# Kernel tuning notes

Hardware: AMD Instinct MI355X
Metric: run time of the kernel (lower is better)

## Reference

```python
import jax, jax.numpy as jnp
import numpy as np

B, T, F, H = 64, 2048, 128, 32  # batch, seq_len, input_features, lstm hidden


def setup_inputs() -> dict:
    key = jax.random.key(0)
    ks = jax.random.split(key, 4)
    X = jax.random.normal(ks[0], (B, T, F), dtype=jnp.float32)
    # combined gate weights, order (i, f, g, o) as in flax.linen.LSTMCell
    Wx = jax.random.normal(ks[1], (F, 4 * H), dtype=jnp.float32) / np.float32(np.sqrt(F))
    Wh = jax.random.normal(ks[2], (H, 4 * H), dtype=jnp.float32) / np.float32(np.sqrt(H))
    b = jnp.zeros((4 * H,), dtype=jnp.float32)
    Wd = jax.random.normal(ks[3], (H, 1), dtype=jnp.float32) / np.float32(np.sqrt(H))
    bd = jnp.zeros((1,), dtype=jnp.float32)
    return {"X": X, "Wx": Wx, "Wh": Wh, "b": b, "Wd": Wd, "bd": bd}


def reference(X, Wx, Wh, b, Wd, bd):
    # Precompute input->gate projections for all timesteps in one GEMM.
    xg = jnp.einsum('btf,fg->btg', X, Wx) + b  # [B, T, 4H]

    def step(carry, xg_t):
        c, h = carry
        g = xg_t + h @ Wh  # [B, 4H]
        i, f, gc, o = jnp.split(g, 4, axis=-1)
        c = jax.nn.sigmoid(f) * c + jax.nn.sigmoid(i) * jnp.tanh(gc)
        h = jax.nn.sigmoid(o) * jnp.tanh(c)
        return (c, h), None

    zeros = jnp.zeros((X.shape[0], H), X.dtype)
    (c_T, h_T), _ = jax.lax.scan(step, (zeros, zeros), jnp.swapaxes(xg, 0, 1))
    # Dense(1) applied to outputs, then last timestep selected == Dense on h_T
    return h_T @ Wd + bd  # [B, 1]
```

## Files before the change

kernel.cpp:

```cpp
#include <hip/hip_runtime.h>
#include <math.h>

#define BB 64
#define TT 2048
#define FF 128
#define HH 32
#define GG 128

#define S1f (-1.4426950408889634f)
#define S2f (-2.8853900817779268f)

typedef _Float16 half2_t __attribute__((ext_vector_type(2)));

__device__ __forceinline__ unsigned h2u(half2_t v) {
    unsigned u; __builtin_memcpy(&u, &v, 4); return u;
}
__device__ __forceinline__ half2_t u2h(unsigned u) {
    half2_t v; __builtin_memcpy(&v, &u, 4); return v;
}
__device__ __forceinline__ half2_t pkrtz(float a, float b) {
    auto r = __builtin_amdgcn_cvt_pkrtz(a, b);
    half2_t v; __builtin_memcpy(&v, &r, 4); return v;
}
__device__ __forceinline__ float rcp_(float x) { return __builtin_amdgcn_rcpf(x); }
__device__ __forceinline__ float exp2_(float x) { return __builtin_amdgcn_exp2f(x); }
__device__ __forceinline__ float fdot2_(half2_t a, half2_t b, float c) {
    return __builtin_amdgcn_fdot2(a, b, c, false);
}

#define DPP_(x, ctrl) \
    ((unsigned)__builtin_amdgcn_mov_dpp((int)(x), (ctrl), 0xF, 0xF, true))
#define CTRL_XOR1 0xB1
#define CTRL_XOR2 0x4E
#define SWZ16_(x) ((unsigned)__builtin_amdgcn_ds_swizzle((int)(x), 0x401F))

#if __has_builtin(__builtin_amdgcn_permlane16_swap)
#define HAVE_PL16 1
#else
#define HAVE_PL16 0
#endif

__device__ __forceinline__ void gather_tree(unsigned v0, unsigned g[16]) {
#if HAVE_PL16
    unsigned v1 = DPP_(v0, CTRL_XOR2);
    auto sw = __builtin_amdgcn_permlane16_swap(v0, v1, false, false);
    unsigned s0 = (unsigned)sw[0], s1 = (unsigned)sw[1];
#else
    unsigned s0 = v0;
    unsigned s1 = SWZ16_(v0);
#endif
    g[0] = s0;                 g[1] = s1;
    g[2]  = DPP_(s0, 0x122);   g[3]  = DPP_(s1, 0x122);
    g[4]  = DPP_(s0, 0x124);   g[5]  = DPP_(s1, 0x124);
    g[6]  = DPP_(s0, 0x126);   g[7]  = DPP_(s1, 0x126);
    g[8]  = DPP_(s0, 0x128);   g[9]  = DPP_(s1, 0x128);
    g[10] = DPP_(s0, 0x12A);   g[11] = DPP_(s1, 0x12A);
    g[12] = DPP_(s0, 0x12C);   g[13] = DPP_(s1, 0x12C);
    g[14] = DPP_(s0, 0x12E);   g[15] = DPP_(s1, 0x12E);
}

__global__ __launch_bounds__(256) void xg_gemm(const float* __restrict__ X,
                                               const float* __restrict__ Wx,
                                               const float* __restrict__ bias,
                                               unsigned* __restrict__ xg2) {
    __shared__ unsigned XLh[64][16];
    __shared__ unsigned WLh[16][128];
    const int tid = threadIdx.x;
    const int row0 = blockIdx.x * 64;
    const int j0 = (tid & 15) * 4;
    const int r0 = (tid >> 4) * 4;

    float acc[4][8];
#pragma unroll
    for (int r = 0; r < 4; ++r)
#pragma unroll
        for (int jj = 0; jj < 8; ++jj) acc[r][jj] = 0.f;

    for (int f0 = 0; f0 < FF; f0 += 32) {
        __syncthreads();
        {
            const int jq = (tid & 31) * 4;
#pragma unroll
            for (int qq = 0; qq < 2; ++qq) {
                const int q = (tid >> 5) + qq * 8;
                float4 wa = *(const float4*)(Wx + (size_t)(f0 + 2 * q) * GG + jq);
                float4 wb = *(const float4*)(Wx + (size_t)(f0 + 2 * q + 1) * GG + jq);
                WLh[q][jq + 0] = h2u(pkrtz(wa.x, wb.x));
                WLh[q][jq + 1] = h2u(pkrtz(wa.y, wb.y));
                WLh[q][jq + 2] = h2u(pkrtz(wa.z, wb.z));
                WLh[q][jq + 3] = h2u(pkrtz(wa.w, wb.w));
            }
        }
        {
            int lin = tid * 4;
            int row = lin >> 5, fi = lin & 31;
            float4 x = *(const float4*)(X + (size_t)(row0 + row) * FF + f0 + fi);
            XLh[row][(fi >> 1) + 0] = h2u(pkrtz(x.x, x.y));
            XLh[row][(fi >> 1) + 1] = h2u(pkrtz(x.z, x.w));
            lin = (tid + 256) * 4;
            row = lin >> 5; fi = lin & 31;
            x = *(const float4*)(X + (size_t)(row0 + row) * FF + f0 + fi);
            XLh[row][(fi >> 1) + 0] = h2u(pkrtz(x.x, x.y));
            XLh[row][(fi >> 1) + 1] = h2u(pkrtz(x.z, x.w));
        }
        __syncthreads();
#pragma unroll 4
        for (int q = 0; q < 16; ++q) {
            half2_t xv[4];
#pragma unroll
            for (int r = 0; r < 4; ++r) xv[r] = u2h(XLh[r0 + r][q]);
            uint4 w0 = *(uint4*)&WLh[q][j0];
            uint4 w1 = *(uint4*)&WLh[q][j0 + 64];
            unsigned wj[8] = {w0.x, w0.y, w0.z, w0.w, w1.x, w1.y, w1.z, w1.w};
#pragma unroll
            for (int r = 0; r < 4; ++r)
#pragma unroll
                for (int jj = 0; jj < 8; ++jj)
                    acc[r][jj] = fdot2_(xv[r], u2h(wj[jj]), acc[r][jj]);
        }
    }
    const int b  = row0 >> 11;
    const int t0 = (row0 & 2047) + r0;
#pragma unroll
    for (int jj = 0; jj < 4; ++jj) {
        const int j = j0 + jj;
        const float bX = bias[j];
        const float bY = bias[j + 64];
        const float sY = (j < 32) ? S2f : S1f;
        uint4 o;
        o.x = h2u(pkrtz((acc[0][jj] + bX) * S1f, (acc[0][jj + 4] + bY) * sY));
        o.y = h2u(pkrtz((acc[1][jj] + bX) * S1f, (acc[1][jj + 4] + bY) * sY));
        o.z = h2u(pkrtz((acc[2][jj] + bX) * S1f, (acc[2][jj + 4] + bY) * sY));
        o.w = h2u(pkrtz((acc[3][jj] + bX) * S1f, (acc[3][jj + 4] + bY) * sY));
        *(uint4*)(xg2 + (size_t)(b * 64 + j) * TT + t0) = o;
    }
}

__global__ __launch_bounds__(64) void lstm_rec(const unsigned* __restrict__ xg2,
                                               const float* __restrict__ Wh,
                                               const float* __restrict__ Wd,
                                               const float* __restrict__ bd,
                                               float* __restrict__ out) {
    const int l = threadIdx.x;
    const int m = l & 31;
    const bool lo = (l < HH);
    const int b = blockIdx.x;

    unsigned iv[16];
    gather_tree((unsigned)m, iv);

    const float scx = S1f;
    const float scy = lo ? S2f : S1f;
    half2_t whx[16], why[16];
#pragma unroll
    for (int r = 0; r < 16; ++r) {
        const int p  = (int)(iv[r] & 31u);
        const int p2 = p ^ 1;
        whx[r] = pkrtz(Wh[p * GG + l] * scx,       Wh[p2 * GG + l] * scx);
        why[r] = pkrtz(Wh[p * GG + l + 64] * scy,  Wh[p2 * GG + l + 64] * scy);
    }

    const float A1 = lo ? 2.f : 1.f;
    const float B1 = lo ? -1.f : 0.f;

    float h = 0.f;
    float c = 0.f;

    const unsigned* pX = xg2 + (size_t)(b * 64 + l) * TT;

    uint4 cur = *(const uint4*)(pX);
    uint4 nxt = *(const uint4*)(pX + 4);

    auto step = [&](unsigned w) __attribute__((always_inline)) {
        half2_t xv = u2h(w);
        float xi = (float)xv[0];
        float xy = (float)xv[1];
        unsigned hn = DPP_(__float_as_uint(h), CTRL_XOR1);
        unsigned g0 = h2u(pkrtz(h, __uint_as_float(hn)));
        unsigned g[16];
        gather_tree(g0, g);
        float ax[4] = {xi, 0.f, 0.f, 0.f};
        float ay[4] = {xy, 0.f, 0.f, 0.f};
#pragma unroll
        for (int r = 0; r < 16; ++r) {
            half2_t hp = u2h(g[r]);
            ax[r & 3] = fdot2_(hp, whx[r], ax[r & 3]);
            ay[r & 3] = fdot2_(hp, why[r], ay[r & 3]);
        }
        float a0 = (ax[0] + ax[1]) + (ax[2] + ax[3]);
        float a1 = (ay[0] + ay[1]) + (ay[2] + ay[3]);
        float act0 = rcp_(1.f + exp2_(a0));
        float act1 = fmaf(A1, rcp_(1.f + exp2_(a1)), B1);
        auto sw0 = __builtin_amdgcn_permlane32_swap(__float_as_uint(act0),
                                                    __float_as_uint(act0), false, false);
        auto sw1 = __builtin_amdgcn_permlane32_swap(__float_as_uint(act1),
                                                    __float_as_uint(act1), false, false);
        float i_all = __uint_as_float(sw0[0]);
        float f_all = __uint_as_float(sw0[1]);
        float g_all = __uint_as_float(sw1[0]);
        float o_all = __uint_as_float(sw1[1]);
        c = fmaf(f_all, c, i_all * g_all);
        float tc = fmaf(2.f, rcp_(1.f + exp2_(c * S2f)), -1.f);
        h = o_all * tc;
    };

#pragma unroll 1
    for (int t4 = 0; t4 < TT; t4 += 4) {
        uint4 u = cur;
        cur = nxt;
        if (t4 + 8 < TT) nxt = *(const uint4*)(pX + t4 + 8);
        step(u.x);
        step(u.y);
        step(u.z);
        step(u.w);
    }

    float contrib = h * Wd[m];
#pragma unroll
    for (int off = 32; off >= 1; off >>= 1)
        contrib += __shfl_xor(contrib, off, 64);
    if (l == 0) out[b] = fmaf(0.5f, contrib, bd[0]);
}

extern "C" void kernel_launch(void* const* d_in, const int* in_sizes, int n_in,
                              void* d_out, int out_size, void* d_ws, size_t ws_size,
                              hipStream_t stream) {
    const float* X    = (const float*)d_in[0];
    const float* Wx   = (const float*)d_in[1];
    const float* Wh   = (const float*)d_in[2];
    const float* bias = (const float*)d_in[3];
    const float* Wd   = (const float*)d_in[4];
    const float* bd   = (const float*)d_in[5];
    float* out = (float*)d_out;
    unsigned* xg2 = (unsigned*)d_ws;

    hipLaunchKernelGGL(xg_gemm, dim3((BB * TT) / 64), dim3(256), 0, stream,
                       X, Wx, bias, xg2);
    hipLaunchKernelGGL(lstm_rec, dim3(BB), dim3(64), 0, stream,
                       xg2, Wh, Wd, bd, out);
}
```

Baseline: 454.5 us.

## Interleave two independent batch recurrences per wavefront to hide dependency latency

Each wavefront now advances two batch elements' LSTM recurrences together, and the launch uses half as many blocks. The two chains' DPP shuffles, dot products, transcendentals and permlane swaps are interleaved, so the latency of each serial step can overlap with the other chain's independent work. Empty inline-asm register barriers are added to pin the instruction order against compiler rescheduling. The cost is more VGPRs and twice the work per step for each wave, with only 32 waves running on a device that has many CUs.

Result: slower. 756.0 us (+66.3%).

```diff
diff --git a/kernel.cpp b/kernel.cpp
--- a/kernel.cpp
+++ b/kernel.cpp
@@ -39,6 +39,12 @@
 #else
 #define HAVE_PL16 0
 #endif
+
+#define LAD2(a, b) asm volatile("" : "+v"(a), "+v"(b))
+#define LAD4(a, b, c, d) asm volatile("" : "+v"(a), "+v"(b), "+v"(c), "+v"(d))
+#define LAD8(a, b, c, d, e, f, g, h) \
+    asm volatile("" : "+v"(a), "+v"(b), "+v"(c), "+v"(d), \
+                      "+v"(e), "+v"(f), "+v"(g), "+v"(h))
 
 __device__ __forceinline__ void gather_tree(unsigned v0, unsigned g[16]) {
 #if HAVE_PL16
@@ -144,7 +150,7 @@
     const int l = threadIdx.x;
     const int m = l & 31;
     const bool lo = (l < HH);
-    const int b = blockIdx.x;
+    const int b0 = blockIdx.x * 2;
 
     unsigned iv[16];
     gather_tree((unsigned)m, iv);
@@ -163,63 +169,156 @@
     const float A1 = lo ? 2.f : 1.f;
     const float B1 = lo ? -1.f : 0.f;
 
-    float h = 0.f;
-    float c = 0.f;
-
-    const unsigned* pX = xg2 + (size_t)(b * 64 + l) * TT;
-
-    uint4 cur = *(const uint4*)(pX);
-    uint4 nxt = *(const uint4*)(pX + 4);
-
-    auto step = [&](unsigned w) __attribute__((always_inline)) {
-        half2_t xv = u2h(w);
-        float xi = (float)xv[0];
-        float xy = (float)xv[1];
-        unsigned hn = DPP_(__float_as_uint(h), CTRL_XOR1);
-        unsigned g0 = h2u(pkrtz(h, __uint_as_float(hn)));
-        unsigned g[16];
-        gather_tree(g0, g);
-        float ax[4] = {xi, 0.f, 0.f, 0.f};
-        float ay[4] = {xy, 0.f, 0.f, 0.f};
-#pragma unroll
-        for (int r = 0; r < 16; ++r) {
-            half2_t hp = u2h(g[r]);
-            ax[r & 3] = fdot2_(hp, whx[r], ax[r & 3]);
-            ay[r & 3] = fdot2_(hp, why[r], ay[r & 3]);
-        }
-        float a0 = (ax[0] + ax[1]) + (ax[2] + ax[3]);
-        float a1 = (ay[0] + ay[1]) + (ay[2] + ay[3]);
-        float act0 = rcp_(1.f + exp2_(a0));
-        float act1 = fmaf(A1, rcp_(1.f + exp2_(a1)), B1);
-        auto sw0 = __builtin_amdgcn_permlane32_swap(__float_as_uint(act0),
-                                                    __float_as_uint(act0), false, false);
-        auto sw1 = __builtin_amdgcn_permlane32_swap(__float_as_uint(act1),
-                                                    __float_as_uint(act1), false, false);
-        float i_all = __uint_as_float(sw0[0]);
-        float f_all = __uint_as_float(sw0[1]);
-        float g_all = __uint_as_float(sw1[0]);
-        float o_all = __uint_as_float(sw1[1]);
-        c = fmaf(f_all, c, i_all * g_all);
-        float tc = fmaf(2.f, rcp_(1.f + exp2_(c * S2f)), -1.f);
-        h = o_all * tc;
+    float hA = 0.f, cA = 0.f, hB = 0.f, cB = 0.f;
+
+    const unsigned* pA = xg2 + (size_t)(b0 * 64 + l) * TT;
+    const unsigned* pB = xg2 + (size_t)((b0 + 1) * 64 + l) * TT;
+
+    uint4 curA = *(const uint4*)(pA);
+    uint4 curB = *(const uint4*)(pB);
+    uint4 nxtA = *(const uint4*)(pA + 4);
+    uint4 nxtB = *(const uint4*)(pB + 4);
+
+    auto dual_step = [&](unsigned wA, unsigned wB)
+        __attribute__((always_inline)) {
+        unsigned hnA = DPP_(__float_as_uint(hA), CTRL_XOR1);
+        unsigned hnB = DPP_(__float_as_uint(hB), CTRL_XOR1);
+        unsigned g0A = h2u(pkrtz(hA, __uint_as_float(hnA)));
+        unsigned g0B = h2u(pkrtz(hB, __uint_as_float(hnB)));
+#if HAVE_PL16
+        unsigned v1A = DPP_(g0A, CTRL_XOR2);
+        unsigned v1B = DPP_(g0B, CTRL_XOR2);
+        auto swA = __builtin_amdgcn_permlane16_swap(g0A, v1A, false, false);
+        auto swB = __builtin_amdgcn_permlane16_swap(g0B, v1B, false, false);
+        unsigned s0A = (unsigned)swA[0], s1A = (unsigned)swA[1];
+        unsigned s0B = (unsigned)swB[0], s1B = (unsigned)swB[1];
+#else
+        unsigned s0A = g0A, s1A = SWZ16_(g0A);
+        unsigned s0B = g0B, s1B = SWZ16_(g0B);
+#endif
+        LAD4(s0A, s1A, s0B, s1B);
+
+        half2_t xvA = u2h(wA);
+        half2_t xvB = u2h(wB);
+        float axA[4] = {(float)xvA[0], 0.f, 0.f, 0.f};
+        float ayA[4] = {(float)xvA[1], 0.f, 0.f, 0.f};
+        float axB[4] = {(float)xvB[0], 0.f, 0.f, 0.f};
+        float ayB[4] = {(float)xvB[1], 0.f, 0.f, 0.f};
+        {
+            half2_t hA0 = u2h(s0A), hA1 = u2h(s1A);
+            half2_t hB0 = u2h(s0B), hB1 = u2h(s1B);
+            axA[0] = fdot2_(hA0, whx[0], axA[0]);
+            axB[0] = fdot2_(hB0, whx[0], axB[0]);
+            ayA[0] = fdot2_(hA0, why[0], ayA[0]);
+            ayB[0] = fdot2_(hB0, why[0], ayB[0]);
+            axA[1] = fdot2_(hA1, whx[1], axA[1]);
+            axB[1] = fdot2_(hB1, whx[1], axB[1]);
+            ayA[1] = fdot2_(hA1, why[1], ayA[1]);
+            ayB[1] = fdot2_(hB1, why[1], ayB[1]);
+        }
+        LAD8(axA[0], ayA[0], axB[0], ayB[0], axA[1], ayA[1], axB[1], ayB[1]);
+
+#define ROR_LEVEL(CTRL, R)                                                  \
+        {                                                                   \
+            unsigned gA0 = DPP_(s0A, (CTRL));                               \
+            unsigned gA1 = DPP_(s1A, (CTRL));                               \
+            unsigned gB0 = DPP_(s0B, (CTRL));                               \
+            unsigned gB1 = DPP_(s1B, (CTRL));                               \
+            axA[(R) & 3] = fdot2_(u2h(gA0), whx[(R)], axA[(R) & 3]);        \
+            axB[(R) & 3] = fdot2_(u2h(gB0), whx[(R)], axB[(R) & 3]);        \
+            ayA[(R) & 3] = fdot2_(u2h(gA0), why[(R)], ayA[(R) & 3]);        \
+            ayB[(R) & 3] = fdot2_(u2h(gB0), why[(R)], ayB[(R) & 3]);        \
+            axA[((R) + 1) & 3] = fdot2_(u2h(gA1), whx[(R) + 1], axA[((R) + 1) & 3]); \
+            axB[((R) + 1) & 3] = fdot2_(u2h(gB1), whx[(R) + 1], axB[((R) + 1) & 3]); \
+            ayA[((R) + 1) & 3] = fdot2_(u2h(gA1), why[(R) + 1], ayA[((R) + 1) & 3]); \
+            ayB[((R) + 1) & 3] = fdot2_(u2h(gB1), why[(R) + 1], ayB[((R) + 1) & 3]); \
+        }
+
+        ROR_LEVEL(0x122, 2)
+        ROR_LEVEL(0x124, 4)
+        LAD8(axA[0], ayA[1], axB[0], ayB[1], axA[2], ayA[3], axB[2], ayB[3]);
+        ROR_LEVEL(0x126, 6)
+        ROR_LEVEL(0x128, 8)
+        LAD8(axA[0], ayA[1], axB[0], ayB[1], axA[2], ayA[3], axB[2], ayB[3]);
+        ROR_LEVEL(0x12A, 10)
+        ROR_LEVEL(0x12C, 12)
+        ROR_LEVEL(0x12E, 14)
+        LAD8(axA[0], ayA[1], axB[0], ayB[1], axA[2], ayA[3], axB[2], ayB[3]);
+#undef ROR_LEVEL
+
+        float a0A = (axA[0] + axA[1]) + (axA[2] + axA[3]);
+        float a0B = (axB[0] + axB[1]) + (axB[2] + axB[3]);
+        float a1A = (ayA[0] + ayA[1]) + (ayA[2] + ayA[3]);
+        float a1B = (ayB[0] + ayB[1]) + (ayB[2] + ayB[3]);
+        LAD4(a0A, a1A, a0B, a1B);
+
+        float e0A = exp2_(a0A);
+        float e0B = exp2_(a0B);
+        float e1A = exp2_(a1A);
+        float e1B = exp2_(a1B);
+        LAD4(e0A, e1A, e0B, e1B);
+        float act0A = rcp_(1.f + e0A);
+        float act0B = rcp_(1.f + e0B);
+        float act1A = fmaf(A1, rcp_(1.f + e1A), B1);
+        float act1B = fmaf(A1, rcp_(1.f + e1B), B1);
+        LAD4(act0A, act1A, act0B, act1B);
+
+        auto sw0A = __builtin_amdgcn_permlane32_swap(__float_as_uint(act0A),
+                                                     __float_as_uint(act0A), false, false);
+        auto sw0B = __builtin_amdgcn_permlane32_swap(__float_as_uint(act0B),
+                                                     __float_as_uint(act0B), false, false);
+        auto sw1A = __builtin_amdgcn_permlane32_swap(__float_as_uint(act1A),
+                                                     __float_as_uint(act1A), false, false);
+        auto sw1B = __builtin_amdgcn_permlane32_swap(__float_as_uint(act1B),
+                                                     __float_as_uint(act1B), false, false);
+        float iA = __uint_as_float(sw0A[0]);
+        float fA = __uint_as_float(sw0A[1]);
+        float gA = __uint_as_float(sw1A[0]);
+        float oA = __uint_as_float(sw1A[1]);
+        float iB = __uint_as_float(sw0B[0]);
+        float fB = __uint_as_float(sw0B[1]);
+        float gB = __uint_as_float(sw1B[0]);
+        float oB = __uint_as_float(sw1B[1]);
+        LAD8(iA, fA, gA, oA, iB, fB, gB, oB);
+        cA = fmaf(fA, cA, iA * gA);
+        cB = fmaf(fB, cB, iB * gB);
+        LAD2(cA, cB);
+        float ecA = exp2_(cA * S2f);
+        float ecB = exp2_(cB * S2f);
+        LAD2(ecA, ecB);
+        float tcA = fmaf(2.f, rcp_(1.f + ecA), -1.f);
+        float tcB = fmaf(2.f, rcp_(1.f + ecB), -1.f);
+        hA = oA * tcA;
+        hB = oB * tcB;
+        LAD4(hA, cA, hB, cB);
     };
 
 #pragma unroll 1
     for (int t4 = 0; t4 < TT; t4 += 4) {
-        uint4 u = cur;
-        cur = nxt;
-        if (t4 + 8 < TT) nxt = *(const uint4*)(pX + t4 + 8);
-        step(u.x);
-        step(u.y);
-        step(u.z);
-        step(u.w);
-    }
-
-    float contrib = h * Wd[m];
-#pragma unroll
-    for (int off = 32; off >= 1; off >>= 1)
-        contrib += __shfl_xor(contrib, off, 64);
-    if (l == 0) out[b] = fmaf(0.5f, contrib, bd[0]);
+        uint4 uA = curA, uB = curB;
+        curA = nxtA; curB = nxtB;
+        if (t4 + 8 < TT) {
+            nxtA = *(const uint4*)(pA + t4 + 8);
+            nxtB = *(const uint4*)(pB + t4 + 8);
+        }
+        dual_step(uA.x, uB.x);
+        dual_step(uA.y, uB.y);
+        dual_step(uA.z, uB.z);
+        dual_step(uA.w, uB.w);
+    }
+
+    const float wd = Wd[m];
+    float ca = hA * wd;
+    float cb = hB * wd;
+#pragma unroll
+    for (int off = 32; off >= 1; off >>= 1) {
+        ca += __shfl_xor(ca, off, 64);
+        cb += __shfl_xor(cb, off, 64);
+    }
+    if (l == 0) {
+        out[b0]     = fmaf(0.5f, ca, bd[0]);
+        out[b0 + 1] = fmaf(0.5f, cb, bd[0]);
+    }
 }
 
 extern "C" void kernel_launch(void* const* d_in, const int* in_sizes, int n_in,
@@ -236,6 +335,6 @@
 
     hipLaunchKernelGGL(xg_gemm, dim3((BB * TT) / 64), dim3(256), 0, stream,
                        X, Wx, bias, xg2);
-    hipLaunchKernelGGL(lstm_rec, dim3(BB), dim3(64), 0, stream,
+    hipLaunchKernelGGL(lstm_rec, dim3(BB / 2), dim3(64), 0, stream,
                        xg2, Wh, Wd, bd, out);
 }
```

## Fuse input GEMM and LSTM recurrence with flag-based producer/consumer tiling

Applied to the files above, without the earlier changes.

Merges the two launches into one kernel. Blocks 0-63 act as producers, each computing the input projection for one batch row in 32 time tiles and publishing a per-tile flag with release semantics. Blocks 64-127 run the recurrence and acquire-poll the next tile's flag before consuming it, so the GEMM overlaps the serial scan instead of finishing first. The catch is a memset per call and the risk of deadlock if consumer blocks get scheduled ahead of producers; producers also use only 64 blocks, which lowers GEMM parallelism.

Result: slower. 596.0 us (+31.1%).

```diff
diff --git a/kernel.cpp b/kernel.cpp
--- a/kernel.cpp
+++ b/kernel.cpp
@@ -6,6 +6,8 @@
 #define FF 128
 #define HH 32
 #define GG 128
+#define NTILE 32
+#define FLAG_OFF (48u * 1024u * 1024u)
 
 #define S1f (-1.4426950408889634f)
 #define S2f (-2.8853900817779268f)
@@ -59,92 +61,110 @@
     g[14] = DPP_(s0, 0x12E);   g[15] = DPP_(s1, 0x12E);
 }
 
-__global__ __launch_bounds__(256) void xg_gemm(const float* __restrict__ X,
-                                               const float* __restrict__ Wx,
-                                               const float* __restrict__ bias,
-                                               unsigned* __restrict__ xg2) {
-    __shared__ unsigned XLh[64][16];
-    __shared__ unsigned WLh[16][128];
-    const int tid = threadIdx.x;
-    const int row0 = blockIdx.x * 64;
-    const int j0 = (tid & 15) * 4;
-    const int r0 = (tid >> 4) * 4;
-
-    float acc[4][8];
-#pragma unroll
-    for (int r = 0; r < 4; ++r)
-#pragma unroll
-        for (int jj = 0; jj < 8; ++jj) acc[r][jj] = 0.f;
-
-    for (int f0 = 0; f0 < FF; f0 += 32) {
-        __syncthreads();
-        {
-            const int jq = (tid & 31) * 4;
-#pragma unroll
-            for (int qq = 0; qq < 2; ++qq) {
-                const int q = (tid >> 5) + qq * 8;
-                float4 wa = *(const float4*)(Wx + (size_t)(f0 + 2 * q) * GG + jq);
-                float4 wb = *(const float4*)(Wx + (size_t)(f0 + 2 * q + 1) * GG + jq);
-                WLh[q][jq + 0] = h2u(pkrtz(wa.x, wb.x));
-                WLh[q][jq + 1] = h2u(pkrtz(wa.y, wb.y));
-                WLh[q][jq + 2] = h2u(pkrtz(wa.z, wb.z));
-                WLh[q][jq + 3] = h2u(pkrtz(wa.w, wb.w));
+__device__ __forceinline__ void waitflag(int* f) {
+    while (__hip_atomic_load(f, __ATOMIC_ACQUIRE, __HIP_MEMORY_SCOPE_AGENT) == 0)
+        __builtin_amdgcn_s_sleep(2);
+}
+
+__global__ __launch_bounds__(256) void lstm_fused2(const float* __restrict__ X,
+                                                   const float* __restrict__ Wx,
+                                                   const float* __restrict__ Wh,
+                                                   const float* __restrict__ bias,
+                                                   const float* __restrict__ Wd,
+                                                   const float* __restrict__ bd,
+                                                   float* __restrict__ out,
+                                                   unsigned* __restrict__ xg2,
+                                                   int* __restrict__ flags) {
+    const int bid = blockIdx.x;
+
+    if (bid < BB) {
+        __shared__ unsigned XLh[64][16];
+        __shared__ unsigned WLh[16][128];
+        const int tid = threadIdx.x;
+        const int b = bid;
+        const int j0 = (tid & 15) * 4;
+        const int r0 = (tid >> 4) * 4;
+
+        for (int tile = 0; tile < NTILE; ++tile) {
+            const int trow0 = tile * 64;
+            float acc[4][8];
+#pragma unroll
+            for (int r = 0; r < 4; ++r)
+#pragma unroll
+                for (int jj = 0; jj < 8; ++jj) acc[r][jj] = 0.f;
+
+            for (int f0 = 0; f0 < FF; f0 += 32) {
+                __syncthreads();
+                {
+                    const int jq = (tid & 31) * 4;
+#pragma unroll
+                    for (int qq = 0; qq < 2; ++qq) {
+                        const int q = (tid >> 5) + qq * 8;
+                        float4 wa = *(const float4*)(Wx + (size_t)(f0 + 2 * q) * GG + jq);
+                        float4 wb = *(const float4*)(Wx + (size_t)(f0 + 2 * q + 1) * GG + jq);
+                        WLh[q][jq + 0] = h2u(pkrtz(wa.x, wb.x));
+                        WLh[q][jq + 1] = h2u(pkrtz(wa.y, wb.y));
+                        WLh[q][jq + 2] = h2u(pkrtz(wa.z, wb.z));
+                        WLh[q][jq + 3] = h2u(pkrtz(wa.w, wb.w));
+                    }
+                }
+                {
+                    int lin = tid * 4;
+                    int row = lin >> 5, fi = lin & 31;
+                    float4 x = *(const float4*)(X + ((size_t)b * TT + trow0 + row) * FF + f0 + fi);
+                    XLh[row][(fi >> 1) + 0] = h2u(pkrtz(x.x, x.y));
+                    XLh[row][(fi >> 1) + 1] = h2u(pkrtz(x.z, x.w));
+                    lin = (tid + 256) * 4;
+                    row = lin >> 5; fi = lin & 31;
+                    x = *(const float4*)(X + ((size_t)b * TT + trow0 + row) * FF + f0 + fi);
+                    XLh[row][(fi >> 1) + 0] = h2u(pkrtz(x.x, x.y));
+                    XLh[row][(fi >> 1) + 1] = h2u(pkrtz(x.z, x.w));
+                }
+                __syncthreads();
+#pragma unroll 4
+                for (int q = 0; q < 16; ++q) {
+                    half2_t xv[4];
+#pragma unroll
+                    for (int r = 0; r < 4; ++r) xv[r] = u2h(XLh[r0 + r][q]);
+                    uint4 w0 = *(uint4*)&WLh[q][j0];
+                    uint4 w1 = *(uint4*)&WLh[q][j0 + 64];
+                    unsigned wj[8] = {w0.x, w0.y, w0.z, w0.w, w1.x, w1.y, w1.z, w1.w};
+#pragma unroll
+                    for (int r = 0; r < 4; ++r)
+#pragma unroll
+                        for (int jj = 0; jj < 8; ++jj)
+                            acc[r][jj] = fdot2_(xv[r], u2h(wj[jj]), acc[r][jj]);
+                }
             }
+            const int t0 = trow0 + r0;
+#pragma unroll
+            for (int jj = 0; jj < 4; ++jj) {
+                const int j = j0 + jj;
+                const float bX = bias[j];
+                const float bY = bias[j + 64];
+                const float sY = (j < 32) ? S2f : S1f;
+                uint4 o;
+                o.x = h2u(pkrtz((acc[0][jj] + bX) * S1f, (acc[0][jj + 4] + bY) * sY));
+                o.y = h2u(pkrtz((acc[1][jj] + bX) * S1f, (acc[1][jj + 4] + bY) * sY));
+                o.z = h2u(pkrtz((acc[2][jj] + bX) * S1f, (acc[2][jj + 4] + bY) * sY));
+                o.w = h2u(pkrtz((acc[3][jj] + bX) * S1f, (acc[3][jj + 4] + bY) * sY));
+                *(uint4*)(xg2 + (size_t)(b * 64 + j) * TT + t0) = o;
+            }
+            __threadfence();
+            __syncthreads();
+            if (tid == 0)
+                __hip_atomic_store(&flags[b * NTILE + tile], 1,
+                                   __ATOMIC_RELEASE, __HIP_MEMORY_SCOPE_AGENT);
         }
-        {
-            int lin = tid * 4;
-            int row = lin >> 5, fi = lin & 31;
-            float4 x = *(const float4*)(X + (size_t)(row0 + row) * FF + f0 + fi);
-            XLh[row][(fi >> 1) + 0] = h2u(pkrtz(x.x, x.y));
-            XLh[row][(fi >> 1) + 1] = h2u(pkrtz(x.z, x.w));
-            lin = (tid + 256) * 4;
-            row = lin >> 5; fi = lin & 31;
-            x = *(const float4*)(X + (size_t)(row0 + row) * FF + f0 + fi);
-            XLh[row][(fi >> 1) + 0] = h2u(pkrtz(x.x, x.y));
-            XLh[row][(fi >> 1) + 1] = h2u(pkrtz(x.z, x.w));
-        }
-        __syncthreads();
-#pragma unroll 4
-        for (int q = 0; q < 16; ++q) {
-            half2_t xv[4];
-#pragma unroll
-            for (int r = 0; r < 4; ++r) xv[r] = u2h(XLh[r0 + r][q]);
-            uint4 w0 = *(uint4*)&WLh[q][j0];
-            uint4 w1 = *(uint4*)&WLh[q][j0 + 64];
-            unsigned wj[8] = {w0.x, w0.y, w0.z, w0.w, w1.x, w1.y, w1.z, w1.w};
-#pragma unroll
-            for (int r = 0; r < 4; ++r)
-#pragma unroll
-                for (int jj = 0; jj < 8; ++jj)
-                    acc[r][jj] = fdot2_(xv[r], u2h(wj[jj]), acc[r][jj]);
-        }
+        return;
     }
-    const int b  = row0 >> 11;
-    const int t0 = (row0 & 2047) + r0;
-#pragma unroll
-    for (int jj = 0; jj < 4; ++jj) {
-        const int j = j0 + jj;
-        const float bX = bias[j];
-        const float bY = bias[j + 64];
-        const float sY = (j < 32) ? S2f : S1f;
-        uint4 o;
-        o.x = h2u(pkrtz((acc[0][jj] + bX) * S1f, (acc[0][jj + 4] + bY) * sY));
-        o.y = h2u(pkrtz((acc[1][jj] + bX) * S1f, (acc[1][jj + 4] + bY) * sY));
-        o.z = h2u(pkrtz((acc[2][jj] + bX) * S1f, (acc[2][jj + 4] + bY) * sY));
-        o.w = h2u(pkrtz((acc[3][jj] + bX) * S1f, (acc[3][jj + 4] + bY) * sY));
-        *(uint4*)(xg2 + (size_t)(b * 64 + j) * TT + t0) = o;
-    }
-}
-
-__global__ __launch_bounds__(64) void lstm_rec(const unsigned* __restrict__ xg2,
-                                               const float* __restrict__ Wh,
-                                               const float* __restrict__ Wd,
-                                               const float* __restrict__ bd,
-                                               float* __restrict__ out) {
+
+    if (threadIdx.x >= 64) return;
     const int l = threadIdx.x;
     const int m = l & 31;
     const bool lo = (l < HH);
-    const int b = blockIdx.x;
+    const int b = bid - BB;
+    int* myflags = flags + b * NTILE;
 
     unsigned iv[16];
     gather_tree((unsigned)m, iv);
@@ -163,11 +183,11 @@
     const float A1 = lo ? 2.f : 1.f;
     const float B1 = lo ? -1.f : 0.f;
 
-    float h = 0.f;
-    float c = 0.f;
+    float h = 0.f, c = 0.f;
 
     const unsigned* pX = xg2 + (size_t)(b * 64 + l) * TT;
 
+    waitflag(myflags);
     uint4 cur = *(const uint4*)(pX);
     uint4 nxt = *(const uint4*)(pX + 4);
 
@@ -204,15 +224,19 @@
         h = o_all * tc;
     };
 
+    for (int k = 0; k < NTILE; ++k) {
+        waitflag(myflags + (k + 1 < NTILE ? k + 1 : NTILE - 1));
 #pragma unroll 1
-    for (int t4 = 0; t4 < TT; t4 += 4) {
-        uint4 u = cur;
-        cur = nxt;
-        if (t4 + 8 < TT) nxt = *(const uint4*)(pX + t4 + 8);
-        step(u.x);
-        step(u.y);
-        step(u.z);
-        step(u.w);
+        for (int g4 = 0; g4 < 16; ++g4) {
+            const int t4 = k * 64 + g4 * 4;
+            uint4 u = cur;
+            cur = nxt;
+            if (t4 + 8 < TT) nxt = *(const uint4*)(pX + t4 + 8);
+            step(u.x);
+            step(u.y);
+            step(u.z);
+            step(u.w);
+        }
     }
 
     float contrib = h * Wd[m];
@@ -233,9 +257,9 @@
     const float* bd   = (const float*)d_in[5];
     float* out = (float*)d_out;
     unsigned* xg2 = (unsigned*)d_ws;
-
-    hipLaunchKernelGGL(xg_gemm, dim3((BB * TT) / 64), dim3(256), 0, stream,
-                       X, Wx, bias, xg2);
-    hipLaunchKernelGGL(lstm_rec, dim3(BB), dim3(64), 0, stream,
-                       xg2, Wh, Wd, bd, out);
-}
+    int* flags = (int*)((char*)d_ws + FLAG_OFF);
+
+    hipMemsetAsync(flags, 0, BB * NTILE * sizeof(int), stream);
+    hipLaunchKernelGGL(lstm_fused2, dim3(2 * BB), dim3(256), 0, stream,
+                       X, Wx, Wh, bias, Wd, bd, out, xg2, flags);
+}
```

## Compute recurrent h@Wh with MFMA 16x16x32 instead of DPP gather and fdot2

Applied to the files above, without the earlier changes.

Replaces the per-step DPP/permlane gather tree and 32 fdot2 ops with four ds_bpermute gathers feeding eight MFMA 16x16x32 f16 instructions that cover all 128 gate columns. Wh is preloaded into MFMA B-operand layout, and each lane selects its gate value from the accumulators. This shortens the serial per-timestep dependency chain of ALU ops. In exchange it adds LDS-path bpermute latency, MFMA pipeline latency, and mostly wasted MFMA rows, since only row 0 of each output tile is used.

Result: slower. 487.3 us (+7.2%).

```diff
diff --git a/kernel.cpp b/kernel.cpp
--- a/kernel.cpp
+++ b/kernel.cpp
@@ -11,6 +11,8 @@
 #define S2f (-2.8853900817779268f)
 
 typedef _Float16 half2_t __attribute__((ext_vector_type(2)));
+typedef _Float16 half8_t __attribute__((ext_vector_type(8)));
+typedef float floatx4 __attribute__((ext_vector_type(4)));
 
 __device__ __forceinline__ unsigned h2u(half2_t v) {
     unsigned u; __builtin_memcpy(&u, &v, 4); return u;
@@ -21,6 +23,10 @@
 __device__ __forceinline__ half2_t pkrtz(float a, float b) {
     auto r = __builtin_amdgcn_cvt_pkrtz(a, b);
     half2_t v; __builtin_memcpy(&v, &r, 4); return v;
+}
+__device__ __forceinline__ half8_t mk8(unsigned a, unsigned b, unsigned c, unsigned d) {
+    unsigned v[4] = {a, b, c, d};
+    half8_t r; __builtin_memcpy(&r, v, 16); return r;
 }
 __device__ __forceinline__ float rcp_(float x) { return __builtin_amdgcn_rcpf(x); }
 __device__ __forceinline__ float exp2_(float x) { return __builtin_amdgcn_exp2f(x); }
@@ -31,33 +37,6 @@
 #define DPP_(x, ctrl) \
     ((unsigned)__builtin_amdgcn_mov_dpp((int)(x), (ctrl), 0xF, 0xF, true))
 #define CTRL_XOR1 0xB1
-#define CTRL_XOR2 0x4E
-#define SWZ16_(x) ((unsigned)__builtin_amdgcn_ds_swizzle((int)(x), 0x401F))
-
-#if __has_builtin(__builtin_amdgcn_permlane16_swap)
-#define HAVE_PL16 1
-#else
-#define HAVE_PL16 0
-#endif
-
-__device__ __forceinline__ void gather_tree(unsigned v0, unsigned g[16]) {
-#if HAVE_PL16
-    unsigned v1 = DPP_(v0, CTRL_XOR2);
-    auto sw = __builtin_amdgcn_permlane16_swap(v0, v1, false, false);
-    unsigned s0 = (unsigned)sw[0], s1 = (unsigned)sw[1];
-#else
-    unsigned s0 = v0;
-    unsigned s1 = SWZ16_(v0);
-#endif
-    g[0] = s0;                 g[1] = s1;
-    g[2]  = DPP_(s0, 0x122);   g[3]  = DPP_(s1, 0x122);
-    g[4]  = DPP_(s0, 0x124);   g[5]  = DPP_(s1, 0x124);
-    g[6]  = DPP_(s0, 0x126);   g[7]  = DPP_(s1, 0x126);
-    g[8]  = DPP_(s0, 0x128);   g[9]  = DPP_(s1, 0x128);
-    g[10] = DPP_(s0, 0x12A);   g[11] = DPP_(s1, 0x12A);
-    g[12] = DPP_(s0, 0x12C);   g[13] = DPP_(s1, 0x12C);
-    g[14] = DPP_(s0, 0x12E);   g[15] = DPP_(s1, 0x12E);
-}
 
 __global__ __launch_bounds__(256) void xg_gemm(const float* __restrict__ X,
                                                const float* __restrict__ Wx,
@@ -143,25 +122,33 @@
                                                float* __restrict__ out) {
     const int l = threadIdx.x;
     const int m = l & 31;
+    const int q = l >> 4;
+    const int cl = l & 15;
     const bool lo = (l < HH);
     const int b = blockIdx.x;
 
-    unsigned iv[16];
-    gather_tree((unsigned)m, iv);
-
-    const float scx = S1f;
-    const float scy = lo ? S2f : S1f;
-    half2_t whx[16], why[16];
-#pragma unroll
-    for (int r = 0; r < 16; ++r) {
-        const int p  = (int)(iv[r] & 31u);
-        const int p2 = p ^ 1;
-        whx[r] = pkrtz(Wh[p * GG + l] * scx,       Wh[p2 * GG + l] * scx);
-        why[r] = pkrtz(Wh[p * GG + l + 64] * scy,  Wh[p2 * GG + l + 64] * scy);
-    }
+    unsigned wb[8][4];
+#pragma unroll
+    for (int t = 0; t < 8; ++t) {
+        const int col = 16 * t + cl;
+        const float sc = (col >= 64 && col < 96) ? S2f : S1f;
+#pragma unroll
+        for (int j = 0; j < 4; ++j) {
+            const int k = 8 * q + 2 * j;
+            wb[t][j] = h2u(pkrtz(Wh[(size_t)k * GG + col] * sc,
+                                 Wh[(size_t)(k + 1) * GG + col] * sc));
+        }
+    }
+
+    int ba0 = (8 * q + 0) * 4;
+    int ba1 = (8 * q + 2) * 4;
+    int ba2 = (8 * q + 4) * 4;
+    int ba3 = (8 * q + 6) * 4;
 
     const float A1 = lo ? 2.f : 1.f;
     const float B1 = lo ? -1.f : 0.f;
+    const bool sel16 = (l & 16) != 0;
+    const bool sel32 = (l & 32) != 0;
 
     float h = 0.f;
     float c = 0.f;
@@ -170,27 +157,40 @@
 
     uint4 cur = *(const uint4*)(pX);
     uint4 nxt = *(const uint4*)(pX + 4);
+
+    const floatx4 zz = {0.f, 0.f, 0.f, 0.f};
 
     auto step = [&](unsigned w) __attribute__((always_inline)) {
         half2_t xv = u2h(w);
         float xi = (float)xv[0];
         float xy = (float)xv[1];
+
         unsigned hn = DPP_(__float_as_uint(h), CTRL_XOR1);
-        unsigned g0 = h2u(pkrtz(h, __uint_as_float(hn)));
-        unsigned g[16];
-        gather_tree(g0, g);
-        float ax[4] = {xi, 0.f, 0.f, 0.f};
-        float ay[4] = {xy, 0.f, 0.f, 0.f};
-#pragma unroll
-        for (int r = 0; r < 16; ++r) {
-            half2_t hp = u2h(g[r]);
-            ax[r & 3] = fdot2_(hp, whx[r], ax[r & 3]);
-            ay[r & 3] = fdot2_(hp, why[r], ay[r & 3]);
-        }
-        float a0 = (ax[0] + ax[1]) + (ax[2] + ax[3]);
-        float a1 = (ay[0] + ay[1]) + (ay[2] + ay[3]);
-        float act0 = rcp_(1.f + exp2_(a0));
-        float act1 = fmaf(A1, rcp_(1.f + exp2_(a1)), B1);
+        unsigned hp = h2u(pkrtz(h, __uint_as_float(hn)));
+        unsigned a0 = (unsigned)__builtin_amdgcn_ds_bpermute(ba0, (int)hp);
+        unsigned a1 = (unsigned)__builtin_amdgcn_ds_bpermute(ba1, (int)hp);
+        unsigned a2 = (unsigned)__builtin_amdgcn_ds_bpermute(ba2, (int)hp);
+        unsigned a3 = (unsigned)__builtin_amdgcn_ds_bpermute(ba3, (int)hp);
+        half8_t A = mk8(a0, a1, a2, a3);
+
+        floatx4 acc0 = __builtin_amdgcn_mfma_f32_16x16x32_f16(A, mk8(wb[0][0], wb[0][1], wb[0][2], wb[0][3]), zz, 0, 0, 0);
+        floatx4 acc1 = __builtin_amdgcn_mfma_f32_16x16x32_f16(A, mk8(wb[1][0], wb[1][1], wb[1][2], wb[1][3]), zz, 0, 0, 0);
+        floatx4 acc2 = __builtin_amdgcn_mfma_f32_16x16x32_f16(A, mk8(wb[2][0], wb[2][1], wb[2][2], wb[2][3]), zz, 0, 0, 0);
+        floatx4 acc3 = __builtin_amdgcn_mfma_f32_16x16x32_f16(A, mk8(wb[3][0], wb[3][1], wb[3][2], wb[3][3]), zz, 0, 0, 0);
+        floatx4 acc4 = __builtin_amdgcn_mfma_f32_16x16x32_f16(A, mk8(wb[4][0], wb[4][1], wb[4][2], wb[4][3]), zz, 0, 0, 0);
+        floatx4 acc5 = __builtin_amdgcn_mfma_f32_16x16x32_f16(A, mk8(wb[5][0], wb[5][1], wb[5][2], wb[5][3]), zz, 0, 0, 0);
+        floatx4 acc6 = __builtin_amdgcn_mfma_f32_16x16x32_f16(A, mk8(wb[6][0], wb[6][1], wb[6][2], wb[6][3]), zz, 0, 0, 0);
+        floatx4 acc7 = __builtin_amdgcn_mfma_f32_16x16x32_f16(A, mk8(wb[7][0], wb[7][1], wb[7][2], wb[7][3]), zz, 0, 0, 0);
+
+        float s0a = sel16 ? acc1[0] : acc0[0];
+        float s0b = sel16 ? acc3[0] : acc2[0];
+        float a0v = (sel32 ? s0b : s0a) + xi;
+        float s1a = sel16 ? acc5[0] : acc4[0];
+        float s1b = sel16 ? acc7[0] : acc6[0];
+        float a1v = (sel32 ? s1b : s1a) + xy;
+
+        float act0 = rcp_(1.f + exp2_(a0v));
+        float act1 = fmaf(A1, rcp_(1.f + exp2_(a1v)), B1);
         auto sw0 = __builtin_amdgcn_permlane32_swap(__float_as_uint(act0),
                                                     __float_as_uint(act0), false, false);
         auto sw1 = __builtin_amdgcn_permlane32_swap(__float_as_uint(act1),
```
